# Kernel optimization log

Hardware: AMD Instinct MI355X
Metric: run time of the kernel (lower is better)

The kernel has to match this reference:

```python
import jax, jax.numpy as jnp
import numpy as np

BATCH, SEQ, HID = 2, 384, 128
TABLE = 2 * SEQ + 1  # indices are diff + SEQ, diff in [-(SEQ-1), SEQ-1]


def setup_inputs() -> dict:
    key = jax.random.key(0)
    ks = jax.random.split(key, 8)
    pos_s = jax.random.randint(ks[0], (BATCH, SEQ), 0, SEQ, dtype=jnp.int64 if jax.config.jax_enable_x64 else jnp.int32)
    # span end >= span start, clipped to valid range
    span = jax.random.randint(ks[1], (BATCH, SEQ), 0, 8, dtype=pos_s.dtype)
    pos_e = jnp.minimum(pos_s + span, SEQ - 1)
    return {
        "pos_s": pos_s,
        "pos_e": pos_e,
        "pe_ss": jax.random.normal(ks[2], (TABLE, HID), dtype=jnp.float32),
        "pe_se": jax.random.normal(ks[3], (TABLE, HID), dtype=jnp.float32),
        "pe_es": jax.random.normal(ks[4], (TABLE, HID), dtype=jnp.float32),
        "pe_ee": jax.random.normal(ks[5], (TABLE, HID), dtype=jnp.float32),
        "W": jax.random.normal(ks[6], (HID, 4 * HID), dtype=jnp.float32) * (1.0 / np.sqrt(4 * HID)),
        "b": jnp.zeros((HID,), dtype=jnp.float32),
    }


def reference(pos_s, pos_e, pe_ss, pe_se, pe_es, pe_ee, W, b):
    S = pos_s.shape[1]
    # pairwise relative positions, shifted into table index range: [B, S, S]
    i_ss = pos_s[:, :, None] - pos_s[:, None, :] + S
    i_se = pos_s[:, :, None] - pos_e[:, None, :] + S
    i_es = pos_e[:, :, None] - pos_s[:, None, :] + S
    i_ee = pos_e[:, :, None] - pos_e[:, None, :] + S
    # gather 4 tables -> [B, S, S, H] each, concat -> [B, S, S, 4H]
    pe_4 = jnp.concatenate([pe_ss[i_ss], pe_se[i_se], pe_es[i_es], pe_ee[i_ee]], axis=-1)
    # Linear(4H -> H) + ReLU  (torch Linear: x @ W.T + b)
    rel = jnp.einsum('bqkf,hf->bqkh', pe_4, W) + b
    return jax.nn.relu(rel)
```

## Files before the change

kernel.cpp:

```cpp
#include <hip/hip_runtime.h>

#define BATCH 2
#define SEQ   384
#define HID   128
#define TABLE (2 * SEQ + 1)
#define KPB   8
#define TPB   8

typedef unsigned int  uint32;
typedef unsigned short ushort16;
typedef float  vfloat4 __attribute__((ext_vector_type(4)));
typedef uint32 vuint2  __attribute__((ext_vector_type(2)));


__device__ __forceinline__ float blo(uint32 u) { return __uint_as_float(u << 16); }
__device__ __forceinline__ float bhi(uint32 u) { return __uint_as_float(u & 0xFFFF0000u); }
__device__ __forceinline__ ushort16 f2bf_rn(float f) {
    uint32 u = __float_as_uint(f);
    u += 0x7FFFu + ((u >> 16) & 1u);
    return (ushort16)(u >> 16);
}

__global__ void transpose_w(const float* __restrict__ W, float* __restrict__ Wt) {
    const int idx = blockIdx.x * 256 + threadIdx.x;
    const int h   = idx & (HID - 1);
    const int f   = (idx >> 7) & (HID - 1);
    const int tab = idx >> 14;
    Wt[idx] = W[h * (4 * HID) + tab * HID + f];
}

__global__ void precompute_tables(const float* __restrict__ pe_ss,
                                  const float* __restrict__ pe_se,
                                  const float* __restrict__ pe_es,
                                  const float* __restrict__ pe_ee,
                                  const float* __restrict__ Wt,
                                  const float* __restrict__ b,
                                  ushort16* __restrict__ T) {
    const int t0  = blockIdx.x * TPB;
    const int tab = blockIdx.y;
    const int h   = threadIdx.x;

    const float* pe = (tab == 0) ? pe_ss : (tab == 1) ? pe_se
                    : (tab == 2) ? pe_es : pe_ee;

    const float* pr[TPB];
#pragma unroll
    for (int r = 0; r < TPB; ++r) {
        int tr = t0 + r; if (tr > TABLE - 1) tr = TABLE - 1;
        pr[r] = pe + (size_t)tr * HID;
    }

    float acc[TPB];
    const float binit = (tab == 0) ? b[h] : 0.0f;
#pragma unroll
    for (int r = 0; r < TPB; ++r) acc[r] = binit;

    const float* wcol = Wt + ((size_t)tab * HID) * HID + h;
#pragma unroll 4
    for (int f = 0; f < HID; ++f) {
        const float wf = wcol[(size_t)f * HID];
#pragma unroll
        for (int r = 0; r < TPB; ++r) acc[r] += pr[r][f] * wf;
    }

#pragma unroll
    for (int r = 0; r < TPB; ++r) {
        const int t = t0 + r;
        if (t < TABLE) T[((size_t)tab * TABLE + t) * HID + h] = f2bf_rn(acc[r]);
    }
}

__global__ void gather_fuse(const int* __restrict__ pos_s,
                            const int* __restrict__ pos_e,
                            const ushort16* __restrict__ T,
                            float* __restrict__ out) {
    const int kk = threadIdx.x >> 5;
    const int h4 = threadIdx.x & 31;
    const int k  = blockIdx.x * KPB + kk;
    const int q  = blockIdx.y;
    const int bb = blockIdx.z;

    const int ps_q = pos_s[bb * SEQ + q];
    const int pe_q = pos_e[bb * SEQ + q];
    const int ps_k = pos_s[bb * SEQ + k];
    const int pe_k = pos_e[bb * SEQ + k];

    const vuint2* T2 = (const vuint2*)T;
    const size_t TR = (size_t)TABLE * 32;

    vuint2 a = T2[         (size_t)(ps_q - ps_k + SEQ) * 32 + h4];
    vuint2 c = T2[    TR + (size_t)(ps_q - pe_k + SEQ) * 32 + h4];
    vuint2 d = T2[2 * TR + (size_t)(pe_q - ps_k + SEQ) * 32 + h4];
    vuint2 e = T2[3 * TR + (size_t)(pe_q - pe_k + SEQ) * 32 + h4];

    vfloat4 r;
    r.x = fmaxf(blo(a.x) + blo(c.x) + blo(d.x) + blo(e.x), 0.0f);
    r.y = fmaxf(bhi(a.x) + bhi(c.x) + bhi(d.x) + bhi(e.x), 0.0f);
    r.z = fmaxf(blo(a.y) + blo(c.y) + blo(d.y) + blo(e.y), 0.0f);
    r.w = fmaxf(bhi(a.y) + bhi(c.y) + bhi(d.y) + bhi(e.y), 0.0f);

    vfloat4* op = (vfloat4*)out + (((size_t)bb * SEQ + q) * SEQ + k) * 32 + h4;
    __builtin_nontemporal_store(r, op);
}

extern "C" void kernel_launch(void* const* d_in, const int* in_sizes, int n_in,
                              void* d_out, int out_size, void* d_ws, size_t ws_size,
                              hipStream_t stream) {
    const int*   pos_s = (const int*)d_in[0];
    const int*   pos_e = (const int*)d_in[1];
    const float* pe_ss = (const float*)d_in[2];
    const float* pe_se = (const float*)d_in[3];
    const float* pe_es = (const float*)d_in[4];
    const float* pe_ee = (const float*)d_in[5];
    const float* W     = (const float*)d_in[6];
    const float* b     = (const float*)d_in[7];
    float*       out   = (float*)d_out;

    ushort16* T  = (ushort16*)d_ws;
    float*    Wt = (float*)((char*)d_ws + (size_t)4 * TABLE * HID * sizeof(ushort16));

    transpose_w<<<dim3((4 * HID * HID) / 256), 256, 0, stream>>>(W, Wt);

    precompute_tables<<<dim3((TABLE + TPB - 1) / TPB, 4), HID, 0, stream>>>(
        pe_ss, pe_se, pe_es, pe_ee, Wt, b, T);

    gather_fuse<<<dim3(SEQ / KPB, SEQ, BATCH), 256, 0, stream>>>(
        pos_s, pos_e, T, out);
}
```

Baseline: 193.8 us.

## Use fp32 precomputed tables, stage W in shared memory, drop transpose kernel

```diff
diff --git a/kernel.cpp b/kernel.cpp
--- a/kernel.cpp
+++ b/kernel.cpp
@@ -7,38 +7,26 @@
 #define KPB   8
 #define TPB   8
 
-typedef unsigned int  uint32;
-typedef unsigned short ushort16;
-typedef float  vfloat4 __attribute__((ext_vector_type(4)));
-typedef uint32 vuint2  __attribute__((ext_vector_type(2)));
+typedef float vfloat4 __attribute__((ext_vector_type(4)));
 
-
-__device__ __forceinline__ float blo(uint32 u) { return __uint_as_float(u << 16); }
-__device__ __forceinline__ float bhi(uint32 u) { return __uint_as_float(u & 0xFFFF0000u); }
-__device__ __forceinline__ ushort16 f2bf_rn(float f) {
-    uint32 u = __float_as_uint(f);
-    u += 0x7FFFu + ((u >> 16) & 1u);
-    return (ushort16)(u >> 16);
-}
-
-__global__ void transpose_w(const float* __restrict__ W, float* __restrict__ Wt) {
-    const int idx = blockIdx.x * 256 + threadIdx.x;
-    const int h   = idx & (HID - 1);
-    const int f   = (idx >> 7) & (HID - 1);
-    const int tab = idx >> 14;
-    Wt[idx] = W[h * (4 * HID) + tab * HID + f];
-}
 
 __global__ void precompute_tables(const float* __restrict__ pe_ss,
                                   const float* __restrict__ pe_se,
                                   const float* __restrict__ pe_es,
                                   const float* __restrict__ pe_ee,
-                                  const float* __restrict__ Wt,
+                                  const float* __restrict__ W,
                                   const float* __restrict__ b,
-                                  ushort16* __restrict__ T) {
+                                  float* __restrict__ T) {
+    __shared__ float wl[HID * HID];
+
     const int t0  = blockIdx.x * TPB;
     const int tab = blockIdx.y;
     const int h   = threadIdx.x;
+
+    for (int r = 0; r < HID; ++r) {
+        wl[h * HID + ((h + r) & (HID - 1))] = W[r * (4 * HID) + tab * HID + h];
+    }
+    __syncthreads();
 
     const float* pe = (tab == 0) ? pe_ss : (tab == 1) ? pe_se
                     : (tab == 2) ? pe_es : pe_ee;
@@ -55,10 +43,9 @@
 #pragma unroll
     for (int r = 0; r < TPB; ++r) acc[r] = binit;
 
-    const float* wcol = Wt + ((size_t)tab * HID) * HID + h;
 #pragma unroll 4
     for (int f = 0; f < HID; ++f) {
-        const float wf = wcol[(size_t)f * HID];
+        const float wf = wl[f * HID + ((f + h) & (HID - 1))];
 #pragma unroll
         for (int r = 0; r < TPB; ++r) acc[r] += pr[r][f] * wf;
     }
@@ -66,13 +53,13 @@
 #pragma unroll
     for (int r = 0; r < TPB; ++r) {
         const int t = t0 + r;
-        if (t < TABLE) T[((size_t)tab * TABLE + t) * HID + h] = f2bf_rn(acc[r]);
+        if (t < TABLE) T[((size_t)tab * TABLE + t) * HID + h] = acc[r];
     }
 }
 
 __global__ void gather_fuse(const int* __restrict__ pos_s,
                             const int* __restrict__ pos_e,
-                            const ushort16* __restrict__ T,
+                            const float* __restrict__ T,
                             float* __restrict__ out) {
     const int kk = threadIdx.x >> 5;
     const int h4 = threadIdx.x & 31;
@@ -85,22 +72,27 @@
     const int ps_k = pos_s[bb * SEQ + k];
     const int pe_k = pos_e[bb * SEQ + k];
 
-    const vuint2* T2 = (const vuint2*)T;
+    const int i_ss = ps_q - ps_k + SEQ;
+    const int i_se = ps_q - pe_k + SEQ;
+    const int i_es = pe_q - ps_k + SEQ;
+    const int i_ee = pe_q - pe_k + SEQ;
+
+    const vfloat4* T4 = (const vfloat4*)T;
     const size_t TR = (size_t)TABLE * 32;
 
-    vuint2 a = T2[         (size_t)(ps_q - ps_k + SEQ) * 32 + h4];
-    vuint2 c = T2[    TR + (size_t)(ps_q - pe_k + SEQ) * 32 + h4];
-    vuint2 d = T2[2 * TR + (size_t)(pe_q - ps_k + SEQ) * 32 + h4];
-    vuint2 e = T2[3 * TR + (size_t)(pe_q - pe_k + SEQ) * 32 + h4];
+    const vfloat4 a = T4[         (size_t)i_ss * 32 + h4];
+    const vfloat4 c = T4[    TR + (size_t)i_se * 32 + h4];
+    const vfloat4 d = T4[2 * TR + (size_t)i_es * 32 + h4];
+    const vfloat4 e = T4[3 * TR + (size_t)i_ee * 32 + h4];
 
     vfloat4 r;
-    r.x = fmaxf(blo(a.x) + blo(c.x) + blo(d.x) + blo(e.x), 0.0f);
-    r.y = fmaxf(bhi(a.x) + bhi(c.x) + bhi(d.x) + bhi(e.x), 0.0f);
-    r.z = fmaxf(blo(a.y) + blo(c.y) + blo(d.y) + blo(e.y), 0.0f);
-    r.w = fmaxf(bhi(a.y) + bhi(c.y) + bhi(d.y) + bhi(e.y), 0.0f);
+    r.x = fmaxf(a.x + c.x + d.x + e.x, 0.0f);
+    r.y = fmaxf(a.y + c.y + d.y + e.y, 0.0f);
+    r.z = fmaxf(a.z + c.z + d.z + e.z, 0.0f);
+    r.w = fmaxf(a.w + c.w + d.w + e.w, 0.0f);
 
     vfloat4* op = (vfloat4*)out + (((size_t)bb * SEQ + q) * SEQ + k) * 32 + h4;
-    __builtin_nontemporal_store(r, op);
+    *op = r;
 }
 
 extern "C" void kernel_launch(void* const* d_in, const int* in_sizes, int n_in,
@@ -116,13 +108,10 @@
     const float* b     = (const float*)d_in[7];
     float*       out   = (float*)d_out;
 
-    ushort16* T  = (ushort16*)d_ws;
-    float*    Wt = (float*)((char*)d_ws + (size_t)4 * TABLE * HID * sizeof(ushort16));
-
-    transpose_w<<<dim3((4 * HID * HID) / 256), 256, 0, stream>>>(W, Wt);
+    float* T = (float*)d_ws;
 
     precompute_tables<<<dim3((TABLE + TPB - 1) / TPB, 4), HID, 0, stream>>>(
-        pe_ss, pe_se, pe_es, pe_ee, Wt, b, T);
+        pe_ss, pe_se, pe_es, pe_ee, W, b, T);
 
     gather_fuse<<<dim3(SEQ / KPB, SEQ, BATCH), 256, 0, stream>>>(
         pos_s, pos_e, T, out);
```

Result: slower. 199.1 us (+2.8%).
